# Performance work log

Measured on AMD Instinct MI355X. Metric: run time of the kernel, lower is better.

Reference implementation:

```python
import jax, jax.numpy as jnp
import numpy as np

H, W, CIN = 448, 608, 64
D = (128, 128, 1024)  # depth list from the module
SCALE = 0.02

def setup_inputs() -> dict:
    key = jax.random.key(0)
    ks = jax.random.split(key, 9)
    f32 = jnp.float32
    return {
        "x":  jax.random.normal(ks[0], (1, CIN, H, W), f32),
        "w1": jax.random.normal(ks[1], (D[0], CIN, 3, 3), f32) * SCALE,
        "b1": jax.random.normal(ks[2], (D[0],), f32) * SCALE,
        "w2": jax.random.normal(ks[3], (H, D[1], D[0]), f32) * SCALE,
        "b2": jax.random.normal(ks[4], (H, D[1]), f32) * SCALE,
        "w3": jax.random.normal(ks[5], (H, D[2], D[1]), f32) * SCALE,
        "b3": jax.random.normal(ks[6], (H, D[2]), f32) * SCALE,
        "w4": jax.random.normal(ks[7], (H, 2, D[2]), f32) * SCALE,
        "b4": jax.random.normal(ks[8], (H, 2), f32) * SCALE,
    }

def _lrelu(v):
    return jax.nn.leaky_relu(v, 0.01)  # PyTorch F.leaky_relu default slope

def reference(x, w1, b1, w2, b2, w3, b3, w4, b4):
    # stage_1: 3x3 conv, padding=1, + leaky_relu   -> [B,128,H,W]
    y = jax.lax.conv_general_dilated(
        x, w1, window_strides=(1, 1), padding='SAME',
        dimension_numbers=('NCHW', 'OIHW', 'NCHW'))
    y = _lrelu(y + b1[None, :, None, None])
    # transpose(1,2) + reshape -> grouped 1x1 convs (groups=H) == per-row GEMMs
    y = jnp.transpose(y, (0, 2, 1, 3))                      # [B,H,128,W]
    y = _lrelu(jnp.einsum('bhcw,hdc->bhdw', y, w2) + b2[None, :, :, None])
    y = _lrelu(jnp.einsum('bhcw,hdc->bhdw', y, w3) + b3[None, :, :, None])
    y = jnp.einsum('bhcw,hdc->bhdw', y, w4) + b4[None, :, :, None]  # [B,H,2,W]
    y = jnp.transpose(y, (0, 2, 1, 3))                      # [B,2,H,W]
    out = y[:, 0]
    mask = _lrelu(y[:, 1])   # mask branch      [B,H,W]
    return (out, mask)
```

## Files before the change

kernel.cpp:

```cpp
#include <hip/hip_runtime.h>

#define HH 448
#define WW 608
#define D1 128
#define D2 128
#define D3 1024
#define HWPROD (HH*WW)
#define CONV_LW 306

typedef __bf16 bf16x8 __attribute__((ext_vector_type(8)));
typedef float  f32x4  __attribute__((ext_vector_type(4)));

__device__ inline unsigned short f2bf(float v) {
    __bf16 b = (__bf16)v;
    return __builtin_bit_cast(unsigned short, b);
}

__device__ inline bf16x8 cvt8c(const float* __restrict__ p) {
    f32x4 f0 = *reinterpret_cast<const f32x4*>(p);
    f32x4 f1 = *reinterpret_cast<const f32x4*>(p + 4);
    bf16x8 r;
    r[0]=(__bf16)f0[0]; r[1]=(__bf16)f0[1]; r[2]=(__bf16)f0[2]; r[3]=(__bf16)f0[3];
    r[4]=(__bf16)f1[0]; r[5]=(__bf16)f1[1]; r[6]=(__bf16)f1[2]; r[7]=(__bf16)f1[3];
    return r;
}

__global__ __launch_bounds__(256) void transpose_x_kernel(
    const float* __restrict__ x, unsigned short* __restrict__ xt)
{
    const int pos = blockIdx.x * 256 + threadIdx.x;
    #pragma unroll
    for (int c8 = 0; c8 < 8; ++c8) {
        bf16x8 r;
        #pragma unroll
        for (int j = 0; j < 8; ++j)
            r[j] = (__bf16)x[(size_t)(c8 * 8 + j) * HWPROD + pos];
        *reinterpret_cast<bf16x8*>(xt + (size_t)pos * 64 + c8 * 8) = r;
    }
}

__global__ __launch_bounds__(256) void convert_w1_kernel(
    const float* __restrict__ w1, unsigned short* __restrict__ w1t)
{
    const int idx = blockIdx.x * 256 + threadIdx.x;
    if (idx >= 9 * D1 * 64) return;
    const int tap = idx / (D1 * 64);
    const int rem = idx - tap * (D1 * 64);
    const int d = rem >> 6, c = rem & 63;
    w1t[idx] = f2bf(w1[(d * 64 + c) * 9 + tap]);
}

__global__ __launch_bounds__(512) void conv_kernel(
    const unsigned short* __restrict__ xt, const unsigned short* __restrict__ w1t,
    const float* __restrict__ b1, unsigned short* __restrict__ y1)
{
    __shared__ __align__(16) unsigned char lds[3 * CONV_LW * 128];
    const int h      = blockIdx.y;
    const int wstart = blockIdx.x * 304;
    const int tid  = threadIdx.x;
    const int lane = tid & 63, wv = tid >> 6;
    const int l15 = lane & 15, lg = lane >> 4;
    const int wd = wv >> 2, wn = wv & 3;
    const int d0 = wd * 64;
    const int start = wn * 5;
    const int cnt   = (wn == 3) ? 4 : 5;

    for (int s = tid; s < 3 * CONV_LW * 8; s += 512) {
        const int slot = s & 7;
        const int rw   = s >> 3;
        const int ri   = rw / CONV_LW;
        const int wl   = rw - ri * CONV_LW;
        const int hs   = h + ri - 1;
        const int gw   = wstart + wl - 1;
        uint4 val = {0u, 0u, 0u, 0u};
        if ((unsigned)hs < (unsigned)HH && (unsigned)gw < (unsigned)WW)
            val = *reinterpret_cast<const uint4*>(xt + ((size_t)hs * WW + gw) * 64 + slot * 8);
        const int dslot = slot ^ (rw & 7);
        *reinterpret_cast<uint4*>(&lds[(size_t)rw * 128 + dslot * 16]) = val;
    }
    __syncthreads();

    f32x4 acc[5][4] = {};

    #pragma unroll
    for (int tap = 0; tap < 9; ++tap) {
        const int ty = tap / 3, tx = tap - ty * 3;
        bf16x8 a[4][2];
        #pragma unroll
        for (int mf = 0; mf < 4; ++mf)
            #pragma unroll
            for (int kc = 0; kc < 2; ++kc)
                a[mf][kc] = *reinterpret_cast<const bf16x8*>(
                    w1t + ((size_t)(tap * D1 + d0 + mf * 16 + l15)) * 64 + kc * 32 + lg * 8);
        #pragma unroll
        for (int f = 0; f < 5; ++f) {
            if (f < cnt) {
                const int col = (start + f) * 16 + l15;
                const int row = ty * CONV_LW + col + tx;
                bf16x8 b[2];
                #pragma unroll
                for (int kc = 0; kc < 2; ++kc) {
                    const int sl = (kc * 4 + lg) ^ (row & 7);
                    b[kc] = *reinterpret_cast<const bf16x8*>(&lds[(size_t)row * 128 + sl * 16]);
                }
                #pragma unroll
                for (int mf = 0; mf < 4; ++mf)
                    #pragma unroll
                    for (int kc = 0; kc < 2; ++kc)
                        acc[f][mf] = __builtin_amdgcn_mfma_f32_16x16x32_bf16(
                            a[mf][kc], b[kc], acc[f][mf], 0, 0, 0);
            }
        }
    }

    f32x4 b1v[4];
    #pragma unroll
    for (int mf = 0; mf < 4; ++mf)
        b1v[mf] = *reinterpret_cast<const f32x4*>(b1 + d0 + mf * 16 + lg * 4);

    #pragma unroll
    for (int f = 0; f < 5; ++f) {
        if (f < cnt) {
            const int w = wstart + (start + f) * 16 + l15;
            #pragma unroll
            for (int mf = 0; mf < 4; ++mf) {
                #pragma unroll
                for (int r = 0; r < 4; ++r) {
                    float v = acc[f][mf][r] + b1v[mf][r];
                    v = fmaxf(v, 0.01f * v);
                    y1[((size_t)h * WW + w) * D1 + d0 + mf * 16 + lg * 4 + r] = f2bf(v);
                }
            }
        }
    }
}

__global__ __launch_bounds__(512) void gemm2_kernel(
    const unsigned short* __restrict__ y1, const float* __restrict__ w2,
    const float* __restrict__ b2, unsigned short* __restrict__ y2)
{
    __shared__ __align__(16) unsigned char lds[WW * 256];
    const int h = blockIdx.x;
    const int tid = threadIdx.x;
    const int lane = tid & 63, wv = tid >> 6;
    const int l15 = lane & 15, lg = lane >> 4;
    const int e0 = wv * 16;

    {
        const unsigned char* src = reinterpret_cast<const unsigned char*>(y1 + (size_t)h * WW * D1);
        #pragma unroll
        for (int i = 0; i < 19; ++i) {
            const int byte = (i * 512 + tid) * 16;
            const int row  = byte >> 8;
            const int slot = (byte >> 4) & 15;
            uint4 val = *reinterpret_cast<const uint4*>(src + byte);
            const int dst = row * 256 + ((slot ^ (row & 7)) << 4);
            *reinterpret_cast<uint4*>(&lds[dst]) = val;
        }
    }

    bf16x8 a[4];
    #pragma unroll
    for (int kc = 0; kc < 4; ++kc)
        a[kc] = cvt8c(w2 + ((size_t)h * D2 + e0 + l15) * D1 + kc * 32 + lg * 8);
    f32x4 b2v = *reinterpret_cast<const f32x4*>(b2 + (size_t)h * D2 + e0 + lg * 4);

    __syncthreads();

    for (int nf = 0; nf < 38; ++nf) {
        const int w = nf * 16 + l15;
        bf16x8 b[4];
        #pragma unroll
        for (int kc = 0; kc < 4; ++kc) {
            const int sl = (kc * 4 + lg) ^ (w & 7);
            b[kc] = *reinterpret_cast<const bf16x8*>(&lds[(size_t)w * 256 + sl * 16]);
        }
        f32x4 t = {};
        #pragma unroll
        for (int kc = 0; kc < 4; ++kc)
            t = __builtin_amdgcn_mfma_f32_16x16x32_bf16(a[kc], b[kc], t, 0, 0, 0);
        #pragma unroll
        for (int r = 0; r < 4; ++r) {
            float v = t[r] + b2v[r];
            v = fmaxf(v, 0.01f * v);
            y2[((size_t)h * WW + w) * D2 + e0 + lg * 4 + r] = f2bf(v);
        }
    }
}

__global__ __launch_bounds__(512) void gemm3_kernel(
    const unsigned short* __restrict__ y2, const float* __restrict__ w3,
    const float* __restrict__ b3, const float* __restrict__ w4,
    const float* __restrict__ b4, float* __restrict__ out)
{
    __shared__ __align__(16) unsigned char lds[WW * 256 + 2 * WW * 4];
    float* pk = reinterpret_cast<float*>(&lds[WW * 256]);
    const int h = blockIdx.x;
    const int tid = threadIdx.x;
    const int lane = tid & 63, wv = tid >> 6;
    const int l15 = lane & 15, lg = lane >> 4;
    const int e0 = wv * 128;

    for (int i = tid; i < 2 * WW; i += 512) pk[i] = 0.f;

    {
        const unsigned char* src = reinterpret_cast<const unsigned char*>(y2 + (size_t)h * WW * D2);
        #pragma unroll
        for (int i = 0; i < 19; ++i) {
            const int byte = (i * 512 + tid) * 16;
            const int row  = byte >> 8;
            const int slot = (byte >> 4) & 15;
            uint4 val = *reinterpret_cast<const uint4*>(src + byte);
            const int dst = row * 256 + ((slot ^ (row & 7)) << 4);
            *reinterpret_cast<uint4*>(&lds[dst]) = val;
        }
    }
    __syncthreads();

    for (int mt = 0; mt < 2; ++mt) {
        const int e64 = e0 + mt * 64;
        bf16x8 a[4][4];
        #pragma unroll
        for (int mf = 0; mf < 4; ++mf)
            #pragma unroll
            for (int kc = 0; kc < 4; ++kc)
                a[mf][kc] = cvt8c(w3 + ((size_t)h * D3 + e64 + mf * 16 + l15) * D2 + kc * 32 + lg * 8);
        f32x4 b3v[4], w40[4], w41[4];
        #pragma unroll
        for (int mf = 0; mf < 4; ++mf) {
            b3v[mf] = *reinterpret_cast<const f32x4*>(b3 + (size_t)h * D3 + e64 + mf * 16 + lg * 4);
            w40[mf] = *reinterpret_cast<const f32x4*>(w4 + (size_t)h * 2 * D3 + e64 + mf * 16 + lg * 4);
            w41[mf] = *reinterpret_cast<const f32x4*>(w4 + (size_t)h * 2 * D3 + D3 + e64 + mf * 16 + lg * 4);
        }

        for (int nf = 0; nf < 38; ++nf) {
            const int w = nf * 16 + l15;
            bf16x8 b[4];
            #pragma unroll
            for (int kc = 0; kc < 4; ++kc) {
                const int sl = (kc * 4 + lg) ^ (w & 7);
                b[kc] = *reinterpret_cast<const bf16x8*>(&lds[(size_t)w * 256 + sl * 16]);
            }
            float p0 = 0.f, p1 = 0.f;
            #pragma unroll
            for (int mf = 0; mf < 4; ++mf) {
                f32x4 t = {};
                #pragma unroll
                for (int kc = 0; kc < 4; ++kc)
                    t = __builtin_amdgcn_mfma_f32_16x16x32_bf16(a[mf][kc], b[kc], t, 0, 0, 0);
                #pragma unroll
                for (int r = 0; r < 4; ++r) {
                    float v = t[r] + b3v[mf][r];
                    v = fmaxf(v, 0.01f * v);
                    p0 = fmaf(w40[mf][r], v, p0);
                    p1 = fmaf(w41[mf][r], v, p1);
                }
            }
            p0 += __shfl_xor(p0, 16); p0 += __shfl_xor(p0, 32);
            p1 += __shfl_xor(p1, 16); p1 += __shfl_xor(p1, 32);
            if (lane < 16) {
                atomicAdd(&pk[w], p0);
                atomicAdd(&pk[WW + w], p1);
            }
        }
    }
    __syncthreads();

    const float bb0 = b4[h * 2 + 0], bb1 = b4[h * 2 + 1];
    for (int i = tid; i < WW; i += 512) {
        float s0 = pk[i] + bb0;
        float s1 = pk[WW + i] + bb1;
        out[(size_t)h * WW + i] = s0;
        out[(size_t)HWPROD + (size_t)h * WW + i] = fmaxf(s1, 0.01f * s1);
    }
}

extern "C" void kernel_launch(void* const* d_in, const int* in_sizes, int n_in,
                              void* d_out, int out_size, void* d_ws, size_t ws_size,
                              hipStream_t stream) {
    const float* x  = (const float*)d_in[0];
    const float* w1 = (const float*)d_in[1];
    const float* b1 = (const float*)d_in[2];
    const float* w2 = (const float*)d_in[3];
    const float* b2 = (const float*)d_in[4];
    const float* w3 = (const float*)d_in[5];
    const float* b3 = (const float*)d_in[6];
    const float* w4 = (const float*)d_in[7];
    const float* b4 = (const float*)d_in[8];
    float* out = (float*)d_out;

    char* ws = (char*)d_ws;
    size_t off = 0;
    unsigned short* y1 = (unsigned short*)(ws + off); off += (size_t)HWPROD * D1 * 2;
    char* regionB = ws + off; off += (size_t)HWPROD * D2 * 2;
    unsigned short* xt = (unsigned short*)regionB;
    unsigned short* y2 = (unsigned short*)regionB;
    unsigned short* w1t = (unsigned short*)(ws + off); off += (size_t)9 * D1 * 64 * 2;

    transpose_x_kernel<<<HWPROD / 256, 256, 0, stream>>>(x, xt);
    convert_w1_kernel<<<(9 * D1 * 64 + 255) / 256, 256, 0, stream>>>(w1, w1t);

    conv_kernel <<<dim3(2, HH), 512, 0, stream>>>(xt, w1t, b1, y1);
    gemm2_kernel<<<HH, 512, 0, stream>>>(y1, w2, b2, y2);
    gemm3_kernel<<<HH, 512, 0, stream>>>(y2, w3, b3, w4, b4, out);
}
```

Measured before the change: 309.2 us.

## Split conv and row GEMM kernels into half-width tiles for more blocks

The conv kernel now covers 152 columns per block instead of 304, and the gemm2/gemm3 kernels each handle half a row (304 columns) instead of a full row. This doubles the grid sizes, halves LDS per block, and sets launch bounds requesting 4 blocks per CU to raise occupancy. Epilogue stores are packed into 64-bit ushort4 writes, and a block-index remap interleaves rows and halves. In exchange, gemm3 reloads w3 weights from global memory twice as often per row, and the conv halo overhead grows.

New measurement: 474.2 us. +53.4%, slower.

```diff
diff --git a/kernel.cpp b/kernel.cpp
--- a/kernel.cpp
+++ b/kernel.cpp
@@ -6,7 +6,7 @@
 #define D2 128
 #define D3 1024
 #define HWPROD (HH*WW)
-#define CONV_LW 306
+#define CLW 164
 
 typedef __bf16 bf16x8 __attribute__((ext_vector_type(8)));
 typedef float  f32x4  __attribute__((ext_vector_type(4)));
@@ -50,37 +50,40 @@
     w1t[idx] = f2bf(w1[(d * 64 + c) * 9 + tap]);
 }
 
-__global__ __launch_bounds__(512) void conv_kernel(
+__global__ __launch_bounds__(512, 4) void conv_kernel(
     const unsigned short* __restrict__ xt, const unsigned short* __restrict__ w1t,
     const float* __restrict__ b1, unsigned short* __restrict__ y1)
 {
-    __shared__ __align__(16) unsigned char lds[3 * CONV_LW * 128];
+    __shared__ __align__(16) unsigned char lds[3 * CLW * 128];
     const int h      = blockIdx.y;
-    const int wstart = blockIdx.x * 304;
+    const int wstart = blockIdx.x * 152;
     const int tid  = threadIdx.x;
     const int lane = tid & 63, wv = tid >> 6;
     const int l15 = lane & 15, lg = lane >> 4;
     const int wd = wv >> 2, wn = wv & 3;
     const int d0 = wd * 64;
-    const int start = wn * 5;
-    const int cnt   = (wn == 3) ? 4 : 5;
-
-    for (int s = tid; s < 3 * CONV_LW * 8; s += 512) {
-        const int slot = s & 7;
-        const int rw   = s >> 3;
-        const int ri   = rw / CONV_LW;
-        const int wl   = rw - ri * CONV_LW;
-        const int hs   = h + ri - 1;
-        const int gw   = wstart + wl - 1;
-        uint4 val = {0u, 0u, 0u, 0u};
-        if ((unsigned)hs < (unsigned)HH && (unsigned)gw < (unsigned)WW)
-            val = *reinterpret_cast<const uint4*>(xt + ((size_t)hs * WW + gw) * 64 + slot * 8);
-        const int dslot = slot ^ (rw & 7);
-        *reinterpret_cast<uint4*>(&lds[(size_t)rw * 128 + dslot * 16]) = val;
+    const int start = (wn < 2) ? wn * 3 : 6 + (wn - 2) * 2;
+    const int cnt   = (wn < 2) ? 3 : 2;
+
+    for (int i = 0; i < 8; ++i) {
+        const int s = i * 512 + tid;
+        if (s < 3 * CLW * 8) {
+            const int slot = s & 7;
+            const int rw   = s >> 3;
+            const int ri   = rw / CLW;
+            const int wl   = rw - ri * CLW;
+            const int hs   = h + ri - 1;
+            const int gw   = wstart + wl - 1;
+            uint4 val = {0u, 0u, 0u, 0u};
+            if ((unsigned)hs < (unsigned)HH && (unsigned)gw < (unsigned)WW)
+                val = *reinterpret_cast<const uint4*>(xt + ((size_t)hs * WW + gw) * 64 + slot * 8);
+            const int dslot = slot ^ (rw & 7);
+            *reinterpret_cast<uint4*>(&lds[(size_t)rw * 128 + dslot * 16]) = val;
+        }
     }
     __syncthreads();
 
-    f32x4 acc[5][4] = {};
+    f32x4 acc[3][4] = {};
 
     #pragma unroll
     for (int tap = 0; tap < 9; ++tap) {
@@ -93,10 +96,10 @@
                 a[mf][kc] = *reinterpret_cast<const bf16x8*>(
                     w1t + ((size_t)(tap * D1 + d0 + mf * 16 + l15)) * 64 + kc * 32 + lg * 8);
         #pragma unroll
-        for (int f = 0; f < 5; ++f) {
+        for (int f = 0; f < 3; ++f) {
             if (f < cnt) {
                 const int col = (start + f) * 16 + l15;
-                const int row = ty * CONV_LW + col + tx;
+                const int row = ty * CLW + col + tx;
                 bf16x8 b[2];
                 #pragma unroll
                 for (int kc = 0; kc < 2; ++kc) {
@@ -119,43 +122,60 @@
         b1v[mf] = *reinterpret_cast<const f32x4*>(b1 + d0 + mf * 16 + lg * 4);
 
     #pragma unroll
-    for (int f = 0; f < 5; ++f) {
+    for (int f = 0; f < 3; ++f) {
         if (f < cnt) {
-            const int w = wstart + (start + f) * 16 + l15;
-            #pragma unroll
-            for (int mf = 0; mf < 4; ++mf) {
-                #pragma unroll
-                for (int r = 0; r < 4; ++r) {
-                    float v = acc[f][mf][r] + b1v[mf][r];
-                    v = fmaxf(v, 0.01f * v);
-                    y1[((size_t)h * WW + w) * D1 + d0 + mf * 16 + lg * 4 + r] = f2bf(v);
+            const int wl = (start + f) * 16 + l15;
+            if (wl < 152) {
+                const int w = wstart + wl;
+                #pragma unroll
+                for (int mf = 0; mf < 4; ++mf) {
+                    ushort4 o;
+                    #pragma unroll
+                    for (int r = 0; r < 4; ++r) {
+                        float v = acc[f][mf][r] + b1v[mf][r];
+                        v = fmaxf(v, 0.01f * v);
+                        ((unsigned short*)&o)[r] = f2bf(v);
+                    }
+                    *reinterpret_cast<ushort4*>(
+                        y1 + ((size_t)h * WW + w) * D1 + d0 + mf * 16 + lg * 4) = o;
                 }
             }
         }
     }
 }
 
-__global__ __launch_bounds__(512) void gemm2_kernel(
+__device__ inline void decode_pair(int bid, int& h, int& half) {
+    const int s = bid & 7, j = bid >> 3;
+    half = j & 1;
+    h = (j >> 1) * 8 + s;
+}
+
+__global__ __launch_bounds__(512, 4) void gemm2_kernel(
     const unsigned short* __restrict__ y1, const float* __restrict__ w2,
     const float* __restrict__ b2, unsigned short* __restrict__ y2)
 {
-    __shared__ __align__(16) unsigned char lds[WW * 256];
-    const int h = blockIdx.x;
+    __shared__ __align__(16) unsigned char lds[304 * 256];
+    int h, half;
+    decode_pair(blockIdx.x, h, half);
+    const int wstart = half * 304;
     const int tid = threadIdx.x;
     const int lane = tid & 63, wv = tid >> 6;
     const int l15 = lane & 15, lg = lane >> 4;
     const int e0 = wv * 16;
 
     {
-        const unsigned char* src = reinterpret_cast<const unsigned char*>(y1 + (size_t)h * WW * D1);
-        #pragma unroll
-        for (int i = 0; i < 19; ++i) {
-            const int byte = (i * 512 + tid) * 16;
-            const int row  = byte >> 8;
-            const int slot = (byte >> 4) & 15;
-            uint4 val = *reinterpret_cast<const uint4*>(src + byte);
-            const int dst = row * 256 + ((slot ^ (row & 7)) << 4);
-            *reinterpret_cast<uint4*>(&lds[dst]) = val;
+        const unsigned char* src = reinterpret_cast<const unsigned char*>(
+            y1 + ((size_t)h * WW + wstart) * D1);
+        #pragma unroll
+        for (int i = 0; i < 10; ++i) {
+            const int c16 = i * 512 + tid;
+            if (c16 < 304 * 16) {
+                const int byte = c16 * 16;
+                const int row  = byte >> 8;
+                const int slot = (byte >> 4) & 15;
+                uint4 val = *reinterpret_cast<const uint4*>(src + byte);
+                *reinterpret_cast<uint4*>(&lds[row * 256 + ((slot ^ (row & 7)) << 4)]) = val;
+            }
         }
     }
 
@@ -167,52 +187,60 @@
 
     __syncthreads();
 
-    for (int nf = 0; nf < 38; ++nf) {
-        const int w = nf * 16 + l15;
+    for (int nf = 0; nf < 19; ++nf) {
+        const int wl = nf * 16 + l15;
         bf16x8 b[4];
         #pragma unroll
         for (int kc = 0; kc < 4; ++kc) {
-            const int sl = (kc * 4 + lg) ^ (w & 7);
-            b[kc] = *reinterpret_cast<const bf16x8*>(&lds[(size_t)w * 256 + sl * 16]);
+            const int sl = (kc * 4 + lg) ^ (wl & 7);
+            b[kc] = *reinterpret_cast<const bf16x8*>(&lds[(size_t)wl * 256 + sl * 16]);
         }
         f32x4 t = {};
         #pragma unroll
         for (int kc = 0; kc < 4; ++kc)
             t = __builtin_amdgcn_mfma_f32_16x16x32_bf16(a[kc], b[kc], t, 0, 0, 0);
+        ushort4 o;
         #pragma unroll
         for (int r = 0; r < 4; ++r) {
             float v = t[r] + b2v[r];
             v = fmaxf(v, 0.01f * v);
-            y2[((size_t)h * WW + w) * D2 + e0 + lg * 4 + r] = f2bf(v);
-        }
-    }
-}
-
-__global__ __launch_bounds__(512) void gemm3_kernel(
+            ((unsigned short*)&o)[r] = f2bf(v);
+        }
+        *reinterpret_cast<ushort4*>(
+            y2 + ((size_t)h * WW + wstart + wl) * D2 + e0 + lg * 4) = o;
+    }
+}
+
+__global__ __launch_bounds__(512, 4) void gemm3_kernel(
     const unsigned short* __restrict__ y2, const float* __restrict__ w3,
     const float* __restrict__ b3, const float* __restrict__ w4,
     const float* __restrict__ b4, float* __restrict__ out)
 {
-    __shared__ __align__(16) unsigned char lds[WW * 256 + 2 * WW * 4];
-    float* pk = reinterpret_cast<float*>(&lds[WW * 256]);
-    const int h = blockIdx.x;
+    __shared__ __align__(16) unsigned char lds[304 * 256 + 2 * 304 * 4];
+    float* pk = reinterpret_cast<float*>(&lds[304 * 256]);
+    int h, half;
+    decode_pair(blockIdx.x, h, half);
+    const int wstart = half * 304;
     const int tid = threadIdx.x;
     const int lane = tid & 63, wv = tid >> 6;
     const int l15 = lane & 15, lg = lane >> 4;
     const int e0 = wv * 128;
 
-    for (int i = tid; i < 2 * WW; i += 512) pk[i] = 0.f;
+    for (int i = tid; i < 2 * 304; i += 512) pk[i] = 0.f;
 
     {
-        const unsigned char* src = reinterpret_cast<const unsigned char*>(y2 + (size_t)h * WW * D2);
-        #pragma unroll
-        for (int i = 0; i < 19; ++i) {
-            const int byte = (i * 512 + tid) * 16;
-            const int row  = byte >> 8;
-            const int slot = (byte >> 4) & 15;
-            uint4 val = *reinterpret_cast<const uint4*>(src + byte);
-            const int dst = row * 256 + ((slot ^ (row & 7)) << 4);
-            *reinterpret_cast<uint4*>(&lds[dst]) = val;
+        const unsigned char* src = reinterpret_cast<const unsigned char*>(
+            y2 + ((size_t)h * WW + wstart) * D2);
+        #pragma unroll
+        for (int i = 0; i < 10; ++i) {
+            const int c16 = i * 512 + tid;
+            if (c16 < 304 * 16) {
+                const int byte = c16 * 16;
+                const int row  = byte >> 8;
+                const int slot = (byte >> 4) & 15;
+                uint4 val = *reinterpret_cast<const uint4*>(src + byte);
+                *reinterpret_cast<uint4*>(&lds[row * 256 + ((slot ^ (row & 7)) << 4)]) = val;
+            }
         }
     }
     __syncthreads();
@@ -233,13 +261,13 @@
             w41[mf] = *reinterpret_cast<const f32x4*>(w4 + (size_t)h * 2 * D3 + D3 + e64 + mf * 16 + lg * 4);
         }
 
-        for (int nf = 0; nf < 38; ++nf) {
-            const int w = nf * 16 + l15;
+        for (int nf = 0; nf < 19; ++nf) {
+            const int wl = nf * 16 + l15;
             bf16x8 b[4];
             #pragma unroll
             for (int kc = 0; kc < 4; ++kc) {
-                const int sl = (kc * 4 + lg) ^ (w & 7);
-                b[kc] = *reinterpret_cast<const bf16x8*>(&lds[(size_t)w * 256 + sl * 16]);
+                const int sl = (kc * 4 + lg) ^ (wl & 7);
+                b[kc] = *reinterpret_cast<const bf16x8*>(&lds[(size_t)wl * 256 + sl * 16]);
             }
             float p0 = 0.f, p1 = 0.f;
             #pragma unroll
@@ -259,19 +287,19 @@
             p0 += __shfl_xor(p0, 16); p0 += __shfl_xor(p0, 32);
             p1 += __shfl_xor(p1, 16); p1 += __shfl_xor(p1, 32);
             if (lane < 16) {
-                atomicAdd(&pk[w], p0);
-                atomicAdd(&pk[WW + w], p1);
+                atomicAdd(&pk[wl], p0);
+                atomicAdd(&pk[304 + wl], p1);
             }
         }
     }
     __syncthreads();
 
     const float bb0 = b4[h * 2 + 0], bb1 = b4[h * 2 + 1];
-    for (int i = tid; i < WW; i += 512) {
+    for (int i = tid; i < 304; i += 512) {
         float s0 = pk[i] + bb0;
-        float s1 = pk[WW + i] + bb1;
-        out[(size_t)h * WW + i] = s0;
-        out[(size_t)HWPROD + (size_t)h * WW + i] = fmaxf(s1, 0.01f * s1);
+        float s1 = pk[304 + i] + bb1;
+        out[(size_t)h * WW + wstart + i] = s0;
+        out[(size_t)HWPROD + (size_t)h * WW + wstart + i] = fmaxf(s1, 0.01f * s1);
     }
 }
 
@@ -300,7 +328,7 @@
     transpose_x_kernel<<<HWPROD / 256, 256, 0, stream>>>(x, xt);
     convert_w1_kernel<<<(9 * D1 * 64 + 255) / 256, 256, 0, stream>>>(w1, w1t);
 
-    conv_kernel <<<dim3(2, HH), 512, 0, stream>>>(xt, w1t, b1, y1);
-    gemm2_kernel<<<HH, 512, 0, stream>>>(y1, w2, b2, y2);
-    gemm3_kernel<<<HH, 512, 0, stream>>>(y2, w3, b3, w4, b4, out);
-}
+    conv_kernel <<<dim3(4, HH), 512, 0, stream>>>(xt, w1t, b1, y1);
+    gemm2_kernel<<<896, 512, 0, stream>>>(y1, w2, b2, y2);
+    gemm3_kernel<<<896, 512, 0, stream>>>(y2, w3, b3, w4, b4, out);
+}
```
